# Performance work log

Hardware: AMD Instinct MI355X
Metric: run time of the kernel (lower is better)

## Reference

```python
import jax, jax.numpy as jnp
import numpy as np

N = 100_000      # nodes
E = 1_600_000    # edges (avg degree 16)
C_IN = 32
C_OUT = 32


def setup_inputs() -> dict:
    key = jax.random.key(0)
    ks = jax.random.split(key, 8)
    x = jax.random.normal(ks[0], (N, C_IN), jnp.float32)
    edge_index = jax.random.randint(ks[1], (2, E), 0, N)
    edge_weight = jax.random.uniform(ks[2], (E,), jnp.float32)
    h = jax.random.normal(ks[3], (N, C_OUT), jnp.float32)
    s_in = 1.0 / np.sqrt(C_IN)
    s_out = 1.0 / np.sqrt(C_OUT)
    # 6 ChebConvs (gates z, r, h-tilde; each has an x-conv and an h-conv), K=2
    Wx = jax.random.normal(ks[4], (3, 2, C_IN, C_OUT), jnp.float32) * s_in
    bx = jnp.zeros((3, C_OUT), jnp.float32)
    Wh = jax.random.normal(ks[5], (3, 2, C_OUT, C_OUT), jnp.float32) * s_out
    bh = jnp.zeros((3, C_OUT), jnp.float32)
    Wl = jax.random.normal(ks[6], (C_OUT, 1), jnp.float32) * s_out
    bl = jnp.zeros((1,), jnp.float32)
    return dict(x=x, edge_index=edge_index, edge_weight=edge_weight, h=h,
                Wx=Wx, bx=bx, Wh=Wh, bh=bh, Wl=Wl, bl=bl)


def _cheb(v, W, b, coef, src, dst, n):
    # ChebConv, K=2, sym norm, lambda_max=2:
    #   T0 = v ; T1 = Lhat @ v, Lhat = -D^{-1/2} A D^{-1/2} (zero diagonal)
    t1 = jax.ops.segment_sum(coef[:, None] * v[src], dst, num_segments=n)
    return v @ W[0] + t1 @ W[1] + b


def reference(x, edge_index, edge_weight, h, Wx, bx, Wh, bh, Wl, bl):
    n = x.shape[0]
    src, dst = edge_index[0], edge_index[1]
    deg = jax.ops.segment_sum(edge_weight, src, num_segments=n)
    safe = jnp.where(deg > 0, deg, 1.0)
    dis = jnp.where(deg > 0, jax.lax.rsqrt(safe), 0.0)
    coef = -(dis[src] * edge_weight * dis[dst])  # scaled-Laplacian edge coeffs

    def gate(g, v_x, v_h):
        return (_cheb(v_x, Wx[g], bx[g], coef, src, dst, n)
                + _cheb(v_h, Wh[g], bh[g], coef, src, dst, n))

    z = jax.nn.sigmoid(gate(0, x, h))          # update gate
    r = jax.nn.sigmoid(gate(1, x, h))          # reset gate
    h_tilde = jnp.tanh(gate(2, x, h * r))      # candidate state
    h_new = z * h + (1.0 - z) * h_tilde
    out = jax.nn.softplus(jax.nn.relu(h_new) @ Wl + bl)  # [N, 1]
    return (out, h_new)
```

## Files before the change

kernel.cpp:

```cpp
#include <hip/hip_runtime.h>
#include <math.h>

#define NN 100000
#define NE 1600000
#define C  32
#define CAP 48

#define BSH    8
#define BNODES 256
#define NB     392
#define BCAP   4608
#define EPB    4096

#define WQ_SCALE 32767.0f
#define INV_WQ   (1.0f/32767.0f)
#define DEG_FIX  4194304.0f
#define INV_DEG_FIX (1.0f/4194304.0f)

typedef __attribute__((ext_vector_type(8))) short short8;
typedef __attribute__((ext_vector_type(4))) float floatx4;

__device__ __forceinline__ unsigned rn_bf16(float f) {
    unsigned b = __float_as_uint(f);
    return (b + 0x7fffu + ((b >> 16) & 1u)) >> 16;
}

__device__ __forceinline__ float sigm(float a) { return 1.f / (1.f + expf(-a)); }

__device__ __forceinline__ unsigned enc_edge(int s, float w) {
    int wq = (int)(w * WQ_SCALE + 0.5f);
    wq = wq > 32767 ? 32767 : wq;
    return ((unsigned)s << 15) | (unsigned)wq;
}

__device__ __forceinline__ short8 pack_hi8(uint4 a, uint4 b) {
    short8 v;
    v[0] = (short)(a.x >> 16); v[1] = (short)(a.y >> 16);
    v[2] = (short)(a.z >> 16); v[3] = (short)(a.w >> 16);
    v[4] = (short)(b.x >> 16); v[5] = (short)(b.y >> 16);
    v[6] = (short)(b.z >> 16); v[7] = (short)(b.w >> 16);
    return v;
}
__device__ __forceinline__ short8 pack_lo8(uint4 a, uint4 b) {
    short8 v;
    v[0] = (short)(a.x & 0xffffu); v[1] = (short)(a.y & 0xffffu);
    v[2] = (short)(a.z & 0xffffu); v[3] = (short)(a.w & 0xffffu);
    v[4] = (short)(b.x & 0xffffu); v[5] = (short)(b.y & 0xffffu);
    v[6] = (short)(b.z & 0xffffu); v[7] = (short)(b.w & 0xffffu);
    return v;
}

__global__ __launch_bounds__(1024) void bin_pass(const int* __restrict__ ei,
                                                 const float* __restrict__ w,
                                                 int* __restrict__ gbin_d,
                                                 int* __restrict__ gbin_s,
                                                 uint2* __restrict__ drec,
                                                 unsigned* __restrict__ srec) {
    __shared__ int hd[NB], hs[NB], bd[NB], bs[NB];
    int tid = threadIdx.x;
    for (int i = tid; i < NB; i += 1024) { hd[i] = 0; hs[i] = 0; }
    __syncthreads();
    int e0 = blockIdx.x * EPB;
    int sl[4], dl[4]; float wl[4];
#pragma unroll
    for (int k = 0; k < 4; ++k) {
        int e = e0 + tid + k * 1024;
        if (e < NE) {
            sl[k] = ei[e]; dl[k] = ei[NE + e]; wl[k] = w[e];
            atomicAdd(&hs[sl[k] >> BSH], 1);
            atomicAdd(&hd[dl[k] >> BSH], 1);
        } else { sl[k] = -1; dl[k] = -1; wl[k] = 0.f; }
    }
    __syncthreads();
    for (int i = tid; i < NB; i += 1024) {
        bd[i] = hd[i] ? atomicAdd(&gbin_d[i], hd[i]) : 0;
        bs[i] = hs[i] ? atomicAdd(&gbin_s[i], hs[i]) : 0;
    }
    __syncthreads();
    for (int i = tid; i < NB; i += 1024) { hd[i] = 0; hs[i] = 0; }
    __syncthreads();
#pragma unroll
    for (int k = 0; k < 4; ++k) {
        int s = sl[k], d = dl[k];
        if (d < 0) continue;
        float we = wl[k];
        int dbin = d >> BSH;
        int off = bd[dbin] + atomicAdd(&hd[dbin], 1);
        if (off < BCAP)
            drec[(size_t)dbin * BCAP + off] =
                make_uint2(((unsigned)s << BSH) | (unsigned)(d & (BNODES - 1)),
                           __float_as_uint(we));
        int sbin = s >> BSH;
        int offs = bs[sbin] + atomicAdd(&hs[sbin], 1);
        if (offs < BCAP)
            srec[(size_t)sbin * BCAP + offs] =
                ((unsigned)(s & (BNODES - 1)) << 22) | (unsigned)(we * DEG_FIX);
    }
}

__global__ __launch_bounds__(1024) void bin_build(const uint2* __restrict__ drec,
                                                  const unsigned* __restrict__ srec,
                                                  const int* __restrict__ gbin_d,
                                                  const int* __restrict__ gbin_s,
                                                  unsigned* __restrict__ buckets,
                                                  int* __restrict__ cursor,
                                                  float* __restrict__ dis) {
    __shared__ __align__(16) unsigned lbuck[BNODES * CAP];
    __shared__ int lcur[BNODES];
    __shared__ int ldeg[BNODES];
    int b = blockIdx.x, tid = threadIdx.x;
    if (tid < BNODES) { lcur[tid] = 0; ldeg[tid] = 0; }
    __syncthreads();
    int cnt_d = min(gbin_d[b], BCAP);
    int cnt_s = min(gbin_s[b], BCAP);
    for (int i = tid; i < cnt_d; i += 1024) {
        uint2 r = drec[(size_t)b * BCAP + i];
        int d8 = r.x & (BNODES - 1);
        int s  = (int)(r.x >> BSH);
        int pos = atomicAdd(&lcur[d8], 1);
        if (pos < CAP) lbuck[d8 * CAP + pos] = enc_edge(s, __uint_as_float(r.y));
    }
    for (int i = tid; i < cnt_s; i += 1024) {
        unsigned r = srec[(size_t)b * BCAP + i];
        atomicAdd(&ldeg[r >> 22], (int)(r & 0x3FFFFFu));
    }
    __syncthreads();
    uint4* gb = (uint4*)(buckets + (size_t)b * BNODES * CAP);
    const uint4* lb = (const uint4*)lbuck;
    for (int i = tid; i < BNODES * CAP / 4; i += 1024) gb[i] = lb[i];
    int n = b * BNODES + tid;
    if (tid < BNODES && n < NN) {
        cursor[n] = min(lcur[tid], CAP);
        int di = ldeg[tid];
        dis[n] = di > 0 ? rsqrtf((float)di * INV_DEG_FIX) : 0.f;
    }
}

__global__ __launch_bounds__(256) void build_xh(const float* __restrict__ x,
                                                const float* __restrict__ h,
                                                const float* __restrict__ dis,
                                                unsigned* __restrict__ xh2,
                                                unsigned* __restrict__ xraw2) {
    int t = blockIdx.x * 256 + threadIdx.x;
    if (t >= NN * C) return;
    float d = dis[t >> 5];
    float xv = x[t], hv = h[t];
    xh2[t]   = (rn_bf16(xv * d) << 16) | rn_bf16(hv * d);
    xraw2[t] = (rn_bf16(xv) << 16) | rn_bf16(hv);
}

__global__ __launch_bounds__(256) void agg_xh(const unsigned* __restrict__ buckets,
                                              const int* __restrict__ cursor,
                                              const float* __restrict__ dis,
                                              const unsigned* __restrict__ xh2,
                                              unsigned* __restrict__ agg2) {
    int tid = threadIdx.x;
    int nl = tid >> 5, j = tid & 31;
    int n = blockIdx.x * 8 + nl;
    if (n >= NN) return;
    int cnt = min(cursor[n], CAP);
    float ax0 = 0.f, ax1 = 0.f, ax2 = 0.f, ax3 = 0.f;
    float ah0 = 0.f, ah1 = 0.f, ah2 = 0.f, ah3 = 0.f;
    for (int base = 0; base < cnt; base += 32) {
        int idx = base + j;
        int sv = 0; float cv = 0.f;
        if (idx < cnt) {
            unsigned u = buckets[(size_t)n * CAP + idx];
            sv = (int)(u >> 15);
            cv = (float)(u & 32767u) * INV_WQ;
        }
        int mm = min(32, cnt - base);
        int i2 = 0;
        for (; i2 + 4 <= mm; i2 += 4) {
            int s0 = __shfl(sv, i2 + 0, 32); float c0 = __shfl(cv, i2 + 0, 32);
            int s1 = __shfl(sv, i2 + 1, 32); float c1 = __shfl(cv, i2 + 1, 32);
            int s2 = __shfl(sv, i2 + 2, 32); float c2 = __shfl(cv, i2 + 2, 32);
            int s3 = __shfl(sv, i2 + 3, 32); float c3 = __shfl(cv, i2 + 3, 32);
            unsigned u0 = xh2[(size_t)s0 * C + j];
            unsigned u1 = xh2[(size_t)s1 * C + j];
            unsigned u2 = xh2[(size_t)s2 * C + j];
            unsigned u3 = xh2[(size_t)s3 * C + j];
            ax0 = fmaf(c0, __uint_as_float(u0 & 0xffff0000u), ax0);
            ah0 = fmaf(c0, __uint_as_float(u0 << 16), ah0);
            ax1 = fmaf(c1, __uint_as_float(u1 & 0xffff0000u), ax1);
            ah1 = fmaf(c1, __uint_as_float(u1 << 16), ah1);
            ax2 = fmaf(c2, __uint_as_float(u2 & 0xffff0000u), ax2);
            ah2 = fmaf(c2, __uint_as_float(u2 << 16), ah2);
            ax3 = fmaf(c3, __uint_as_float(u3 & 0xffff0000u), ax3);
            ah3 = fmaf(c3, __uint_as_float(u3 << 16), ah3);
        }
        for (; i2 < mm; ++i2) {
            int s = __shfl(sv, i2, 32); float cf = __shfl(cv, i2, 32);
            unsigned u = xh2[(size_t)s * C + j];
            ax0 = fmaf(cf, __uint_as_float(u & 0xffff0000u), ax0);
            ah0 = fmaf(cf, __uint_as_float(u << 16), ah0);
        }
    }
    float disn = -dis[n];
    float ax = disn * ((ax0 + ax1) + (ax2 + ax3));
    float ah = disn * ((ah0 + ah1) + (ah2 + ah3));
    agg2[(size_t)n * C + j] = (rn_bf16(ax) << 16) | rn_bf16(ah);
}

__global__ __launch_bounds__(256) void gate_mfma(const unsigned* __restrict__ xraw2,
                                                 const unsigned* __restrict__ agg2,
                                                 const float* __restrict__ dis,
                                                 const float* __restrict__ Wx,
                                                 const float* __restrict__ Wh,
                                                 const float* __restrict__ bx,
                                                 const float* __restrict__ bh,
                                                 unsigned* __restrict__ hrz2,
                                                 unsigned short* __restrict__ hr16,
                                                 float* __restrict__ pout) {
    __shared__ __align__(16) unsigned short Bl[20][64][8];
    int tid = threadIdx.x;
    for (int i = tid; i < 20 * 64; i += 256) {
        int f = i >> 6, l = i & 63;
        int t, c;
        if (f < 16) { t = f >> 2; c = f & 3; }
        else        { t = 4 + ((f - 16) >> 1); c = (f - 16) & 1; }
        int g = t >> 1;
        int j = ((t & 1) << 4) + (l & 15);
        int kb = (l >> 4) << 3;
        const float* srcp = (c < 2 ? Wx : Wh) + g * 2048 + (c & 1) * 1024 + j;
        unsigned pk[4];
#pragma unroll
        for (int q = 0; q < 4; ++q) {
            unsigned lo = rn_bf16(srcp[(kb + 2 * q) * 32]);
            unsigned hi = rn_bf16(srcp[(kb + 2 * q + 1) * 32]);
            pk[q] = (hi << 16) | lo;
        }
        *(uint4*)(&Bl[f][l][0]) = make_uint4(pk[0], pk[1], pk[2], pk[3]);
    }

    int lane = tid & 63, wave = tid >> 6;
    int j0 = lane & 15, quad = lane >> 4;
    int tbase = blockIdx.x * 64 + wave * 16;
    int na = tbase + j0;
    short8 A0 = {0,0,0,0,0,0,0,0}, A1 = A0, A2 = A0, A3 = A0;
    if (na < NN) {
        const uint4* px = (const uint4*)(xraw2 + (size_t)na * C + quad * 8);
        uint4 xa = px[0], xb = px[1];
        A0 = pack_hi8(xa, xb);
        A2 = pack_lo8(xa, xb);
        const uint4* pg = (const uint4*)(agg2 + (size_t)na * C + quad * 8);
        uint4 ga = pg[0], gb = pg[1];
        A1 = pack_hi8(ga, gb);
        A3 = pack_lo8(ga, gb);
    }
    __syncthreads();

#define B8(f) (*(const short8*)(&Bl[f][lane][0]))
    floatx4 az0 = {0.f,0.f,0.f,0.f}, az1 = az0, ar0 = az0, ar1 = az0, ap0 = az0, ap1 = az0;
    az0 = __builtin_amdgcn_mfma_f32_16x16x32_bf16(A0, B8(0),  az0, 0, 0, 0);
    az0 = __builtin_amdgcn_mfma_f32_16x16x32_bf16(A1, B8(1),  az0, 0, 0, 0);
    az0 = __builtin_amdgcn_mfma_f32_16x16x32_bf16(A2, B8(2),  az0, 0, 0, 0);
    az0 = __builtin_amdgcn_mfma_f32_16x16x32_bf16(A3, B8(3),  az0, 0, 0, 0);
    az1 = __builtin_amdgcn_mfma_f32_16x16x32_bf16(A0, B8(4),  az1, 0, 0, 0);
    az1 = __builtin_amdgcn_mfma_f32_16x16x32_bf16(A1, B8(5),  az1, 0, 0, 0);
    az1 = __builtin_amdgcn_mfma_f32_16x16x32_bf16(A2, B8(6),  az1, 0, 0, 0);
    az1 = __builtin_amdgcn_mfma_f32_16x16x32_bf16(A3, B8(7),  az1, 0, 0, 0);
    ar0 = __builtin_amdgcn_mfma_f32_16x16x32_bf16(A0, B8(8),  ar0, 0, 0, 0);
    ar0 = __builtin_amdgcn_mfma_f32_16x16x32_bf16(A1, B8(9),  ar0, 0, 0, 0);
    ar0 = __builtin_amdgcn_mfma_f32_16x16x32_bf16(A2, B8(10), ar0, 0, 0, 0);
    ar0 = __builtin_amdgcn_mfma_f32_16x16x32_bf16(A3, B8(11), ar0, 0, 0, 0);
    ar1 = __builtin_amdgcn_mfma_f32_16x16x32_bf16(A0, B8(12), ar1, 0, 0, 0);
    ar1 = __builtin_amdgcn_mfma_f32_16x16x32_bf16(A1, B8(13), ar1, 0, 0, 0);
    ar1 = __builtin_amdgcn_mfma_f32_16x16x32_bf16(A2, B8(14), ar1, 0, 0, 0);
    ar1 = __builtin_amdgcn_mfma_f32_16x16x32_bf16(A3, B8(15), ar1, 0, 0, 0);
    ap0 = __builtin_amdgcn_mfma_f32_16x16x32_bf16(A0, B8(16), ap0, 0, 0, 0);
    ap0 = __builtin_amdgcn_mfma_f32_16x16x32_bf16(A1, B8(17), ap0, 0, 0, 0);
    ap1 = __builtin_amdgcn_mfma_f32_16x16x32_bf16(A0, B8(18), ap1, 0, 0, 0);
    ap1 = __builtin_amdgcn_mfma_f32_16x16x32_bf16(A1, B8(19), ap1, 0, 0, 0);
#undef B8

    float bza = bx[j0]      + bh[j0];
    float bzb = bx[j0 + 16] + bh[j0 + 16];
    float bra = bx[32 + j0] + bh[32 + j0];
    float brb = bx[48 + j0] + bh[48 + j0];
    float bpa = bx[64 + j0] + bh[64 + j0];
    float bpb = bx[80 + j0] + bh[80 + j0];
#pragma unroll
    for (int p = 0; p < 4; ++p) {
        int nr = tbase + quad * 4 + p;
        if (nr >= NN) continue;
        float dn = dis[nr];
        size_t ra = (size_t)nr * C + j0;
        size_t rb = ra + 16;
        float ha = __uint_as_float(xraw2[ra] << 16);
        float hb = __uint_as_float(xraw2[rb] << 16);
        float za  = sigm(az0[p] + bza);
        float zb  = sigm(az1[p] + bzb);
        float rav = sigm(ar0[p] + bra);
        float rbv = sigm(ar1[p] + brb);
        float hra = ha * rav, hrb = hb * rbv;
        hrz2[ra] = (rn_bf16(hra) << 16) | rn_bf16(za);
        hrz2[rb] = (rn_bf16(hrb) << 16) | rn_bf16(zb);
        hr16[ra] = (unsigned short)rn_bf16(dn * hra);
        hr16[rb] = (unsigned short)rn_bf16(dn * hrb);
        pout[ra] = ap0[p] + bpa;
        pout[rb] = ap1[p] + bpb;
    }
}

__global__ __launch_bounds__(256) void final_kernel(const float* __restrict__ h,
                                                    const unsigned* __restrict__ hrz2,
                                                    const float* __restrict__ ph,
                                                    const unsigned* __restrict__ buckets,
                                                    const int* __restrict__ cursor,
                                                    const float* __restrict__ dis,
                                                    const unsigned short* __restrict__ hr16,
                                                    const float* __restrict__ Wh,
                                                    const float* __restrict__ Wl,
                                                    const float* __restrict__ bl,
                                                    float* __restrict__ out,
                                                    float* __restrict__ hnew) {
    __shared__ float sW[2 * 1024];
    __shared__ float sIn[2][8][C];
    int tid = threadIdx.x;
    for (int i = tid; i < 2 * 1024; i += 256) sW[i] = Wh[4096 + i];
    int nl = tid >> 5, j = tid & 31;
    int n = blockIdx.x * 8 + nl;
    if (n >= NN) return;

    int cnt = min(cursor[n], CAP);
    float a0 = 0.f, a1 = 0.f, a2 = 0.f, a3 = 0.f;
    for (int base = 0; base < cnt; base += 32) {
        int idx = base + j;
        int sv = 0; float cv = 0.f;
        if (idx < cnt) {
            unsigned u = buckets[(size_t)n * CAP + idx];
            sv = (int)(u >> 15);
            cv = (float)(u & 32767u) * INV_WQ;
        }
        int mm = min(32, cnt - base);
        int i2 = 0;
        for (; i2 + 4 <= mm; i2 += 4) {
            int s0 = __shfl(sv, i2 + 0, 32); float c0 = __shfl(cv, i2 + 0, 32);
            int s1 = __shfl(sv, i2 + 1, 32); float c1 = __shfl(cv, i2 + 1, 32);
            int s2 = __shfl(sv, i2 + 2, 32); float c2 = __shfl(cv, i2 + 2, 32);
            int s3 = __shfl(sv, i2 + 3, 32); float c3 = __shfl(cv, i2 + 3, 32);
            float v0 = __uint_as_float(((unsigned)hr16[(size_t)s0 * C + j]) << 16);
            float v1 = __uint_as_float(((unsigned)hr16[(size_t)s1 * C + j]) << 16);
            float v2 = __uint_as_float(((unsigned)hr16[(size_t)s2 * C + j]) << 16);
            float v3 = __uint_as_float(((unsigned)hr16[(size_t)s3 * C + j]) << 16);
            a0 = fmaf(c0, v0, a0);
            a1 = fmaf(c1, v1, a1);
            a2 = fmaf(c2, v2, a2);
            a3 = fmaf(c3, v3, a3);
        }
        for (; i2 < mm; ++i2) {
            int s = __shfl(sv, i2, 32); float cf = __shfl(cv, i2, 32);
            a0 = fmaf(cf, __uint_as_float(((unsigned)hr16[(size_t)s * C + j]) << 16), a0);
        }
    }
    float ag = -dis[n] * ((a0 + a1) + (a2 + a3));
    unsigned uz = hrz2[(size_t)n * C + j];
    float hrv = __uint_as_float(uz & 0xffff0000u);
    float zv  = __uint_as_float(uz << 16);
    sIn[0][nl][j] = hrv;
    sIn[1][nl][j] = ag;
    __syncthreads();

    float acc = ph[(size_t)n * C + j];
#pragma unroll
    for (int k = 0; k < C; ++k) {
        int o = k * 32 + j;
        acc = fmaf(sIn[0][nl][k], sW[o], acc);
        acc = fmaf(sIn[1][nl][k], sW[1024 + o], acc);
    }
    float ht = tanhf(acc);
    float hv = h[(size_t)n * C + j];
    float hn = fmaf(zv, hv - ht, ht);
    hnew[(size_t)n * C + j] = hn;
    float p = fmaxf(hn, 0.f) * Wl[j];
#pragma unroll
    for (int off = 16; off; off >>= 1) p += __shfl_down(p, off, 32);
    if (j == 0) {
        float v = p + bl[0];
        out[n] = fmaxf(v, 0.f) + log1pf(expf(-fabsf(v)));
    }
}

extern "C" void kernel_launch(void* const* d_in, const int* in_sizes, int n_in,
                              void* d_out, int out_size, void* d_ws, size_t ws_size,
                              hipStream_t stream) {
    const float* x  = (const float*)d_in[0];
    const int*   ei = (const int*)d_in[1];
    const float* ew = (const float*)d_in[2];
    const float* h  = (const float*)d_in[3];
    const float* Wx = (const float*)d_in[4];
    const float* bx = (const float*)d_in[5];
    const float* Wh = (const float*)d_in[6];
    const float* bh = (const float*)d_in[7];
    const float* Wl = (const float*)d_in[8];
    const float* bl = (const float*)d_in[9];

    float* out  = (float*)d_out;
    float* hnew = out + NN;

    char* ws = (char*)d_ws;
    int*            gbin_d = (int*)ws;
    int*            gbin_s = gbin_d + NB;
    uint2*          drec   = (uint2*)(ws + 4096);
    unsigned*       srec   = (unsigned*)(drec + (size_t)NB * BCAP);
    unsigned*       buckets= srec + (size_t)NB * BCAP;
    int*            cursor = (int*)(buckets + (size_t)NB * BNODES * CAP);
    float*          dis    = (float*)(cursor + NN);
    unsigned*       xh2    = (unsigned*)(dis + NN);
    unsigned*       agg2   = xh2 + (size_t)NN * C;
    float*          pbuf   = (float*)(agg2 + (size_t)NN * C);
    unsigned*       xraw2  = (unsigned*)drec;
    unsigned short* hr16   = (unsigned short*)srec;
    unsigned*       hrz2   = xh2;

    hipMemsetAsync(d_ws, 0, 4096, stream);

    bin_pass    <<<(NE + EPB - 1) / EPB, 1024, 0, stream>>>(ei, ew, gbin_d, gbin_s,
                                                            drec, srec);
    bin_build   <<<NB, 1024, 0, stream>>>(drec, srec, gbin_d, gbin_s,
                                          buckets, cursor, dis);
    build_xh    <<<(NN * C + 255) / 256, 256, 0, stream>>>(x, h, dis, xh2, xraw2);
    agg_xh      <<<(NN + 7) / 8, 256, 0, stream>>>(buckets, cursor, dis, xh2, agg2);
    gate_mfma   <<<(NN + 63) / 64, 256, 0, stream>>>(xraw2, agg2, dis, Wx, Wh,
                                                     bx, bh, hrz2, hr16, pbuf);
    final_kernel<<<(NN + 7) / 8, 256, 0, stream>>>(h, hrz2, pbuf,
                                                   buckets, cursor, dis, hr16,
                                                   Wh, Wl, bl, out, hnew);
}
```

Baseline: 261.3 us.

## Process two channels per lane in gather kernels and stage buckets in LDS

The two gather kernels (agg_xh and final_kernel) now run 16 nodes per block with 16 lanes per node. Each lane handles two channels through wider loads, and each node's bucket list is staged in shared memory instead of being broadcast with warp shuffles. The final kernel repacks the Wh weights as float4 so one shared-memory load feeds both channels. bin_pass also takes more edges per block (7 per thread instead of 4), giving fewer blocks and fewer global bin atomics. The aim is fewer gather instructions and shuffles and better memory-level parallelism, at the cost of more registers and bucket padding.

```diff
diff --git a/kernel.cpp b/kernel.cpp
--- a/kernel.cpp
+++ b/kernel.cpp
@@ -10,7 +10,7 @@
 #define BNODES 256
 #define NB     392
 #define BCAP   4608
-#define EPB    4096
+#define EPB    6272
 
 #define WQ_SCALE 32767.0f
 #define INV_WQ   (1.0f/32767.0f)
@@ -61,11 +61,12 @@
     for (int i = tid; i < NB; i += 1024) { hd[i] = 0; hs[i] = 0; }
     __syncthreads();
     int e0 = blockIdx.x * EPB;
-    int sl[4], dl[4]; float wl[4];
-#pragma unroll
-    for (int k = 0; k < 4; ++k) {
-        int e = e0 + tid + k * 1024;
-        if (e < NE) {
+    int sl[7], dl[7]; float wl[7];
+#pragma unroll
+    for (int k = 0; k < 7; ++k) {
+        int off = tid + k * 1024;
+        int e = e0 + off;
+        if (off < EPB && e < NE) {
             sl[k] = ei[e]; dl[k] = ei[NE + e]; wl[k] = w[e];
             atomicAdd(&hs[sl[k] >> BSH], 1);
             atomicAdd(&hd[dl[k] >> BSH], 1);
@@ -80,7 +81,7 @@
     for (int i = tid; i < NB; i += 1024) { hd[i] = 0; hs[i] = 0; }
     __syncthreads();
 #pragma unroll
-    for (int k = 0; k < 4; ++k) {
+    for (int k = 0; k < 7; ++k) {
         int s = sl[k], d = dl[k];
         if (d < 0) continue;
         float we = wl[k];
@@ -154,52 +155,55 @@
                                               const float* __restrict__ dis,
                                               const unsigned* __restrict__ xh2,
                                               unsigned* __restrict__ agg2) {
+    __shared__ unsigned sbk[16][52];
+    const char* xb = (const char*)xh2;
     int tid = threadIdx.x;
-    int nl = tid >> 5, j = tid & 31;
-    int n = blockIdx.x * 8 + nl;
-    if (n >= NN) return;
+    int nl = tid >> 4, j2 = tid & 15;
+    int n = blockIdx.x * 16 + nl;
     int cnt = min(cursor[n], CAP);
-    float ax0 = 0.f, ax1 = 0.f, ax2 = 0.f, ax3 = 0.f;
-    float ah0 = 0.f, ah1 = 0.f, ah2 = 0.f, ah3 = 0.f;
-    for (int base = 0; base < cnt; base += 32) {
-        int idx = base + j;
-        int sv = 0; float cv = 0.f;
-        if (idx < cnt) {
-            unsigned u = buckets[(size_t)n * CAP + idx];
-            sv = (int)(u >> 15);
-            cv = (float)(u & 32767u) * INV_WQ;
-        }
-        int mm = min(32, cnt - base);
-        int i2 = 0;
-        for (; i2 + 4 <= mm; i2 += 4) {
-            int s0 = __shfl(sv, i2 + 0, 32); float c0 = __shfl(cv, i2 + 0, 32);
-            int s1 = __shfl(sv, i2 + 1, 32); float c1 = __shfl(cv, i2 + 1, 32);
-            int s2 = __shfl(sv, i2 + 2, 32); float c2 = __shfl(cv, i2 + 2, 32);
-            int s3 = __shfl(sv, i2 + 3, 32); float c3 = __shfl(cv, i2 + 3, 32);
-            unsigned u0 = xh2[(size_t)s0 * C + j];
-            unsigned u1 = xh2[(size_t)s1 * C + j];
-            unsigned u2 = xh2[(size_t)s2 * C + j];
-            unsigned u3 = xh2[(size_t)s3 * C + j];
-            ax0 = fmaf(c0, __uint_as_float(u0 & 0xffff0000u), ax0);
-            ah0 = fmaf(c0, __uint_as_float(u0 << 16), ah0);
-            ax1 = fmaf(c1, __uint_as_float(u1 & 0xffff0000u), ax1);
-            ah1 = fmaf(c1, __uint_as_float(u1 << 16), ah1);
-            ax2 = fmaf(c2, __uint_as_float(u2 & 0xffff0000u), ax2);
-            ah2 = fmaf(c2, __uint_as_float(u2 << 16), ah2);
-            ax3 = fmaf(c3, __uint_as_float(u3 & 0xffff0000u), ax3);
-            ah3 = fmaf(c3, __uint_as_float(u3 << 16), ah3);
-        }
-        for (; i2 < mm; ++i2) {
-            int s = __shfl(sv, i2, 32); float cf = __shfl(cv, i2, 32);
-            unsigned u = xh2[(size_t)s * C + j];
-            ax0 = fmaf(cf, __uint_as_float(u & 0xffff0000u), ax0);
-            ah0 = fmaf(cf, __uint_as_float(u << 16), ah0);
-        }
-    }
-    float disn = -dis[n];
-    float ax = disn * ((ax0 + ax1) + (ax2 + ax3));
-    float ah = disn * ((ah0 + ah1) + (ah2 + ah3));
-    agg2[(size_t)n * C + j] = (rn_bf16(ax) << 16) | rn_bf16(ah);
+    int cnt4 = (cnt + 3) & ~3;
+    unsigned brow = (unsigned)n * CAP;
+    for (int i = j2; i < cnt4; i += 16)
+        sbk[nl][i] = (i < cnt) ? buckets[brow + i] : 0u;
+    __syncthreads();
+    unsigned jj = (unsigned)(j2 << 3);
+    float axe0 = 0.f, ahe0 = 0.f, axo0 = 0.f, aho0 = 0.f;
+    float axe1 = 0.f, ahe1 = 0.f, axo1 = 0.f, aho1 = 0.f;
+    for (int i = 0; i < cnt4; i += 4) {
+        unsigned u0 = sbk[nl][i + 0], u1 = sbk[nl][i + 1];
+        unsigned u2 = sbk[nl][i + 2], u3 = sbk[nl][i + 3];
+        unsigned o0 = (u0 >> 8) & 0x00FFFF80u; float c0 = (float)(u0 & 32767u) * INV_WQ;
+        unsigned o1 = (u1 >> 8) & 0x00FFFF80u; float c1 = (float)(u1 & 32767u) * INV_WQ;
+        unsigned o2 = (u2 >> 8) & 0x00FFFF80u; float c2 = (float)(u2 & 32767u) * INV_WQ;
+        unsigned o3 = (u3 >> 8) & 0x00FFFF80u; float c3 = (float)(u3 & 32767u) * INV_WQ;
+        uint2 v0 = *(const uint2*)(xb + (o0 + jj));
+        uint2 v1 = *(const uint2*)(xb + (o1 + jj));
+        uint2 v2 = *(const uint2*)(xb + (o2 + jj));
+        uint2 v3 = *(const uint2*)(xb + (o3 + jj));
+        axe0 = fmaf(c0, __uint_as_float(v0.x & 0xffff0000u), axe0);
+        ahe0 = fmaf(c0, __uint_as_float(v0.x << 16), ahe0);
+        axo0 = fmaf(c0, __uint_as_float(v0.y & 0xffff0000u), axo0);
+        aho0 = fmaf(c0, __uint_as_float(v0.y << 16), aho0);
+        axe1 = fmaf(c1, __uint_as_float(v1.x & 0xffff0000u), axe1);
+        ahe1 = fmaf(c1, __uint_as_float(v1.x << 16), ahe1);
+        axo1 = fmaf(c1, __uint_as_float(v1.y & 0xffff0000u), axo1);
+        aho1 = fmaf(c1, __uint_as_float(v1.y << 16), aho1);
+        axe0 = fmaf(c2, __uint_as_float(v2.x & 0xffff0000u), axe0);
+        ahe0 = fmaf(c2, __uint_as_float(v2.x << 16), ahe0);
+        axo0 = fmaf(c2, __uint_as_float(v2.y & 0xffff0000u), axo0);
+        aho0 = fmaf(c2, __uint_as_float(v2.y << 16), aho0);
+        axe1 = fmaf(c3, __uint_as_float(v3.x & 0xffff0000u), axe1);
+        ahe1 = fmaf(c3, __uint_as_float(v3.x << 16), ahe1);
+        axo1 = fmaf(c3, __uint_as_float(v3.y & 0xffff0000u), axo1);
+        aho1 = fmaf(c3, __uint_as_float(v3.y << 16), aho1);
+    }
+    float dn = -dis[n];
+    float ax_e = dn * (axe0 + axe1), ah_e = dn * (ahe0 + ahe1);
+    float ax_o = dn * (axo0 + axo1), ah_o = dn * (aho0 + aho1);
+    uint2 ov;
+    ov.x = (rn_bf16(ax_e) << 16) | rn_bf16(ah_e);
+    ov.y = (rn_bf16(ax_o) << 16) | rn_bf16(ah_o);
+    *(uint2*)(agg2 + (size_t)n * C + 2 * j2) = ov;
 }
 
 __global__ __launch_bounds__(256) void gate_mfma(const unsigned* __restrict__ xraw2,
@@ -315,68 +319,76 @@
                                                     const float* __restrict__ bl,
                                                     float* __restrict__ out,
                                                     float* __restrict__ hnew) {
-    __shared__ float sW[2 * 1024];
-    __shared__ float sIn[2][8][C];
+    __shared__ __align__(16) float4 sW4[32][16];
+    __shared__ __align__(16) float2 sIn2[16][33];
+    __shared__ unsigned sbk[16][52];
+    const char* hb = (const char*)hr16;
     int tid = threadIdx.x;
-    for (int i = tid; i < 2 * 1024; i += 256) sW[i] = Wh[4096 + i];
-    int nl = tid >> 5, j = tid & 31;
-    int n = blockIdx.x * 8 + nl;
-    if (n >= NN) return;
-
+    for (int i = tid; i < 512; i += 256) {
+        int k = i >> 4, q = i & 15;
+        sW4[k][q] = make_float4(Wh[4096 + k * 32 + 2 * q], Wh[5120 + k * 32 + 2 * q],
+                                Wh[4096 + k * 32 + 2 * q + 1], Wh[5120 + k * 32 + 2 * q + 1]);
+    }
+    int nl = tid >> 4, j2 = tid & 15;
+    int n = blockIdx.x * 16 + nl;
     int cnt = min(cursor[n], CAP);
-    float a0 = 0.f, a1 = 0.f, a2 = 0.f, a3 = 0.f;
-    for (int base = 0; base < cnt; base += 32) {
-        int idx = base + j;
-        int sv = 0; float cv = 0.f;
-        if (idx < cnt) {
-            unsigned u = buckets[(size_t)n * CAP + idx];
-            sv = (int)(u >> 15);
-            cv = (float)(u & 32767u) * INV_WQ;
-        }
-        int mm = min(32, cnt - base);
-        int i2 = 0;
-        for (; i2 + 4 <= mm; i2 += 4) {
-            int s0 = __shfl(sv, i2 + 0, 32); float c0 = __shfl(cv, i2 + 0, 32);
-            int s1 = __shfl(sv, i2 + 1, 32); float c1 = __shfl(cv, i2 + 1, 32);
-            int s2 = __shfl(sv, i2 + 2, 32); float c2 = __shfl(cv, i2 + 2, 32);
-            int s3 = __shfl(sv, i2 + 3, 32); float c3 = __shfl(cv, i2 + 3, 32);
-            float v0 = __uint_as_float(((unsigned)hr16[(size_t)s0 * C + j]) << 16);
-            float v1 = __uint_as_float(((unsigned)hr16[(size_t)s1 * C + j]) << 16);
-            float v2 = __uint_as_float(((unsigned)hr16[(size_t)s2 * C + j]) << 16);
-            float v3 = __uint_as_float(((unsigned)hr16[(size_t)s3 * C + j]) << 16);
-            a0 = fmaf(c0, v0, a0);
-            a1 = fmaf(c1, v1, a1);
-            a2 = fmaf(c2, v2, a2);
-            a3 = fmaf(c3, v3, a3);
-        }
-        for (; i2 < mm; ++i2) {
-            int s = __shfl(sv, i2, 32); float cf = __shfl(cv, i2, 32);
-            a0 = fmaf(cf, __uint_as_float(((unsigned)hr16[(size_t)s * C + j]) << 16), a0);
-        }
-    }
-    float ag = -dis[n] * ((a0 + a1) + (a2 + a3));
-    unsigned uz = hrz2[(size_t)n * C + j];
-    float hrv = __uint_as_float(uz & 0xffff0000u);
-    float zv  = __uint_as_float(uz << 16);
-    sIn[0][nl][j] = hrv;
-    sIn[1][nl][j] = ag;
-    __syncthreads();
-
-    float acc = ph[(size_t)n * C + j];
+    int cnt4 = (cnt + 3) & ~3;
+    unsigned brow = (unsigned)n * CAP;
+    for (int i = j2; i < cnt4; i += 16)
+        sbk[nl][i] = (i < cnt) ? buckets[brow + i] : 0u;
+    __syncthreads();
+    unsigned jj = (unsigned)(j2 << 2);
+    float ae0 = 0.f, ao0 = 0.f, ae1 = 0.f, ao1 = 0.f;
+    for (int i = 0; i < cnt4; i += 4) {
+        unsigned u0 = sbk[nl][i + 0], u1 = sbk[nl][i + 1];
+        unsigned u2 = sbk[nl][i + 2], u3 = sbk[nl][i + 3];
+        unsigned o0 = (u0 >> 9) & 0x007FFFC0u; float c0 = (float)(u0 & 32767u) * INV_WQ;
+        unsigned o1 = (u1 >> 9) & 0x007FFFC0u; float c1 = (float)(u1 & 32767u) * INV_WQ;
+        unsigned o2 = (u2 >> 9) & 0x007FFFC0u; float c2 = (float)(u2 & 32767u) * INV_WQ;
+        unsigned o3 = (u3 >> 9) & 0x007FFFC0u; float c3 = (float)(u3 & 32767u) * INV_WQ;
+        unsigned v0 = *(const unsigned*)(hb + (o0 + jj));
+        unsigned v1 = *(const unsigned*)(hb + (o1 + jj));
+        unsigned v2 = *(const unsigned*)(hb + (o2 + jj));
+        unsigned v3 = *(const unsigned*)(hb + (o3 + jj));
+        ae0 = fmaf(c0, __uint_as_float(v0 << 16), ae0);
+        ao0 = fmaf(c0, __uint_as_float(v0 & 0xffff0000u), ao0);
+        ae1 = fmaf(c1, __uint_as_float(v1 << 16), ae1);
+        ao1 = fmaf(c1, __uint_as_float(v1 & 0xffff0000u), ao1);
+        ae0 = fmaf(c2, __uint_as_float(v2 << 16), ae0);
+        ao0 = fmaf(c2, __uint_as_float(v2 & 0xffff0000u), ao0);
+        ae1 = fmaf(c3, __uint_as_float(v3 << 16), ae1);
+        ao1 = fmaf(c3, __uint_as_float(v3 & 0xffff0000u), ao1);
+    }
+    float dn = -dis[n];
+    float ag_e = dn * (ae0 + ae1);
+    float ag_o = dn * (ao0 + ao1);
+    uint2 uzp = *(const uint2*)(hrz2 + (size_t)n * C + 2 * j2);
+    float hre = __uint_as_float(uzp.x & 0xffff0000u), ze = __uint_as_float(uzp.x << 16);
+    float hro = __uint_as_float(uzp.y & 0xffff0000u), zo = __uint_as_float(uzp.y << 16);
+    sIn2[nl][2 * j2]     = make_float2(hre, ag_e);
+    sIn2[nl][2 * j2 + 1] = make_float2(hro, ag_o);
+    __syncthreads();
+
+    float2 php = *(const float2*)(ph + (size_t)n * C + 2 * j2);
+    float acc_e = php.x, acc_o = php.y;
 #pragma unroll
     for (int k = 0; k < C; ++k) {
-        int o = k * 32 + j;
-        acc = fmaf(sIn[0][nl][k], sW[o], acc);
-        acc = fmaf(sIn[1][nl][k], sW[1024 + o], acc);
-    }
-    float ht = tanhf(acc);
-    float hv = h[(size_t)n * C + j];
-    float hn = fmaf(zv, hv - ht, ht);
-    hnew[(size_t)n * C + j] = hn;
-    float p = fmaxf(hn, 0.f) * Wl[j];
-#pragma unroll
-    for (int off = 16; off; off >>= 1) p += __shfl_down(p, off, 32);
-    if (j == 0) {
+        float2 in = sIn2[nl][k];
+        float4 wp = sW4[k][j2];
+        acc_e = fmaf(in.x, wp.x, acc_e);
+        acc_e = fmaf(in.y, wp.y, acc_e);
+        acc_o = fmaf(in.x, wp.z, acc_o);
+        acc_o = fmaf(in.y, wp.w, acc_o);
+    }
+    float hte = tanhf(acc_e), hto = tanhf(acc_o);
+    float2 hv = *(const float2*)(h + (size_t)n * C + 2 * j2);
+    float hne = fmaf(ze, hv.x - hte, hte);
+    float hno = fmaf(zo, hv.y - hto, hto);
+    *(float2*)(hnew + (size_t)n * C + 2 * j2) = make_float2(hne, hno);
+    float p = fmaxf(hne, 0.f) * Wl[2 * j2] + fmaxf(hno, 0.f) * Wl[2 * j2 + 1];
+#pragma unroll
+    for (int off = 8; off; off >>= 1) p += __shfl_down(p, off, 16);
+    if (j2 == 0) {
         float v = p + bl[0];
         out[n] = fmaxf(v, 0.f) + log1pf(expf(-fabsf(v)));
     }
@@ -421,10 +433,10 @@
     bin_build   <<<NB, 1024, 0, stream>>>(drec, srec, gbin_d, gbin_s,
                                           buckets, cursor, dis);
     build_xh    <<<(NN * C + 255) / 256, 256, 0, stream>>>(x, h, dis, xh2, xraw2);
-    agg_xh      <<<(NN + 7) / 8, 256, 0, stream>>>(buckets, cursor, dis, xh2, agg2);
+    agg_xh      <<<NN / 16, 256, 0, stream>>>(buckets, cursor, dis, xh2, agg2);
     gate_mfma   <<<(NN + 63) / 64, 256, 0, stream>>>(xraw2, agg2, dis, Wx, Wh,
                                                      bx, bh, hrz2, hr16, pbuf);
-    final_kernel<<<(NN + 7) / 8, 256, 0, stream>>>(h, hrz2, pbuf,
-                                                   buckets, cursor, dis, hr16,
-                                                   Wh, Wl, bl, out, hnew);
-}
+    final_kernel<<<NN / 16, 256, 0, stream>>>(h, hrz2, pbuf,
+                                              buckets, cursor, dis, hr16,
+                                              Wh, Wl, bl, out, hnew);
+}
```

New measurement: 260.6 us. About the same (-0.3%).
